# Optimization experiments

Hardware: AMD Instinct MI355X
Metric: run time of the kernel (lower is better)

## Reference

```python
import jax, jax.numpy as jnp
import numpy as np

DIM_X, DIM_Z, D_MODEL, N_HEADS, BATCH = 512, 256, 256, 8, 32


def sinusoidal_pe(seq_len, d_model):
    # standard sinusoidal table, rows indexed by position
    pos = np.arange(seq_len)[:, None].astype(np.float32)
    div = np.exp(np.arange(0, d_model, 2).astype(np.float32) * (-np.log(10000.0) / d_model))
    pe = np.zeros((seq_len, d_model), dtype=np.float32)
    pe[:, 0::2] = np.sin(pos * div)
    pe[:, 1::2] = np.cos(pos * div)
    return jnp.asarray(pe)


def setup_inputs() -> dict:
    key = jax.random.key(0)
    ks = jax.random.split(key, 5)
    state = jax.random.normal(ks[0], (BATCH, D_MODEL, DIM_X), dtype=jnp.float32)
    obs = jax.random.normal(ks[1], (BATCH, D_MODEL, DIM_Z), dtype=jnp.float32)
    Qp = jax.random.uniform(ks[2], (DIM_X, D_MODEL), dtype=jnp.float32)  # torch.rand init
    Wq = jax.random.normal(ks[3], (D_MODEL, D_MODEL), dtype=jnp.float32) / np.sqrt(D_MODEL)
    Wk = jax.random.normal(ks[4], (D_MODEL, D_MODEL), dtype=jnp.float32) / np.sqrt(D_MODEL)
    bq = jnp.zeros((D_MODEL,), dtype=jnp.float32)
    bk = jnp.zeros((D_MODEL,), dtype=jnp.float32)
    return {"state": state, "obs": obs, "Qp": Qp, "Wq": Wq, "bq": bq, "Wk": Wk, "bk": bk}


def reference(state, obs, Qp, Wq, bq, Wk, bk):
    bs, en, dim_x = state.shape
    dim_z = obs.shape[2]
    d_model = Qp.shape[1]
    h = N_HEADS
    hd = d_model // h
    S = dim_x + dim_z

    # mean-center over the ensemble axis
    A = state - jnp.mean(state, axis=1, keepdims=True)   # [bs, en, dim_x]
    Y = obs - jnp.mean(obs, axis=1, keepdims=True)       # [bs, en, dim_z]
    A = jnp.transpose(A, (2, 0, 1))                      # [dim_x, bs, en]
    Y = jnp.transpose(Y, (2, 0, 1))                      # [dim_z, bs, en]

    # positional encoding: batch_first=True quirk -> PE indexed along axis 1 (the bs axis)
    pe = sinusoidal_pe(bs, d_model)[None, :, :]          # [1, bs, d_model]
    query = Qp[:, None, :] + pe                          # [dim_x, bs, d_model] (broadcast of repeat)
    xy = jnp.concatenate([A, Y], axis=0) + pe            # [S, bs, d_model]

    # multi-head attention weights (V / out-proj do not affect returned quantities)
    q = (query @ Wq.T + bq).reshape(dim_x, bs, h, hd)
    k = (xy @ Wk.T + bk).reshape(S, bs, h, hd)
    scores = jnp.einsum('lbhd,sbhd->bhls', q, k) / np.sqrt(hd)  # [bs, h, dim_x, S]

    # fixed structured mask: eye(dim_x) | bottom-padded eye(dim_z)
    p1 = jnp.eye(dim_x, dtype=bool)
    p2 = jnp.concatenate([jnp.zeros((dim_x - dim_z, dim_z), dtype=bool),
                          jnp.eye(dim_z, dtype=bool)], axis=0)
    allow = jnp.concatenate([p1, p2], axis=1)            # [dim_x, S]
    scores = jnp.where(allow[None, None], scores, -jnp.inf)
    atten = jnp.mean(jax.nn.softmax(scores, axis=-1), axis=1)  # average over heads -> [bs, dim_x, S]

    # weighted merge of the ORIGINAL (uncentered) state/obs
    merge = jnp.concatenate([jnp.transpose(state, (0, 2, 1)),
                             jnp.transpose(obs, (0, 2, 1))], axis=1)  # [bs, S, en]
    new_state = jnp.einsum('bls,bse->ble', atten, merge)              # [bs, dim_x, en]
    new_state = jnp.transpose(new_state, (0, 2, 1))                   # [bs, en, dim_x]
    return new_state, atten
```

## Files before the change

kernel.cpp:

```cpp
#include <hip/hip_runtime.h>
#include <stdint.h>
#include <math.h>


#define WS_P    0
#define WS_QWT  8192
#define WS_PQ   73728
#define WS_U    81920
#define WS_V    606208
#define WS_QPT  671744
#define WS_WQT  737280

typedef float vf4 __attribute__((ext_vector_type(4)));
__device__ __forceinline__ void nt_store4(float* p, float x, float y,
                                          float z, float w) {
  vf4 v; v.x = x; v.y = y; v.z = z; v.w = w;
  __builtin_nontemporal_store(v, (vf4*)p);
}

__global__ void __launch_bounds__(256)
k_tr(const float* __restrict__ Qp, const float* __restrict__ Wq,
     float* __restrict__ ws) {
  __shared__ float tile[32][33];
  int bid = blockIdx.x, t = threadIdx.x;
  const float* src; float* dst; int ti;
  if (bid < 64) { src = Qp + 65536; dst = ws + WS_QPT; ti = bid; }
  else          { src = Wq;         dst = ws + WS_WQT; ti = bid - 64; }
  int tr = ti >> 3, tc = ti & 7;
  int c = t & 31, r0 = t >> 5;
  #pragma unroll
  for (int k = 0; k < 4; ++k) {
    int r = r0 + (k << 3);
    tile[r][c] = src[(size_t)(tr * 32 + r) * 256 + tc * 32 + c];
  }
  __syncthreads();
  #pragma unroll
  for (int k = 0; k < 4; ++k) {
    int r = r0 + (k << 3);
    dst[(size_t)(tc * 32 + r) * 256 + tr * 32 + c] = tile[c][r];
  }
}

__global__ void __launch_bounds__(256)
k_pro(const float* __restrict__ Wq, float* __restrict__ ws) {
  int bid = blockIdx.x, t = threadIdx.x;
  __shared__ float lvec[256];
  const float* __restrict__ GT; float* dst;
  if (bid < 256) {
    int d = bid;
    lvec[t] = Wq[(size_t)d * 256 + t];
    GT = ws + WS_QPT; dst = ws + WS_QWT + d * 256;
  } else {
    int b = bid - 256;
    int k2 = t & ~1;
    float div = expf((float)k2 * (-9.210340371976184f / 256.f));
    float a = (float)b * div;
    lvec[t] = (t & 1) ? cosf(a) : sinf(a);
    GT = ws + WS_WQT; dst = ws + WS_PQ + b * 256;
  }
  __syncthreads();
  float acc = 0.f;
  #pragma unroll 8
  for (int e = 0; e < 256; ++e)
    acc += lvec[e] * GT[(e << 8) + t];
  dst[t] = acc;
}

__global__ void __launch_bounds__(256)
k_uv(const float* __restrict__ Wk, const float* __restrict__ bq,
     float* __restrict__ ws) {
  int bid = blockIdx.x, t = threadIdx.x;
  if (bid < 256) {
    int h = bid >> 5, e0 = (bid & 31) << 3;
    __shared__ float wk_s[32][9];
    {
      int d = t >> 3, i = t & 7;
      wk_s[d][i] = Wk[(size_t)(h * 32 + d) * 256 + e0 + i];
    }
    __syncthreads();
    float acc[8] = {0.f, 0.f, 0.f, 0.f, 0.f, 0.f, 0.f, 0.f};
    const float* __restrict__ Qw = ws + WS_QWT + t;
    #pragma unroll 4
    for (int d = 0; d < 32; ++d) {
      float q = Qw[((h << 5) + d) << 8];
      #pragma unroll
      for (int i = 0; i < 8; ++i) acc[i] += wk_s[d][i] * q;
    }
    float* Uh = ws + WS_U + (h << 16) + (size_t)e0 * 256;
    #pragma unroll
    for (int i = 0; i < 8; ++i) Uh[(size_t)i * 256 + t] = acc[i];
  } else {
    int idx = bid - 256, b = idx >> 3, h = idx & 7;
    float acc = 0.f;
#pragma unroll 8
    for (int dd = 0; dd < 32; ++dd) {
      int d = h * 32 + dd;
      acc += (ws[WS_PQ + b * 256 + d] + bq[d]) * Wk[(size_t)d * 256 + t];
    }
    ws[WS_V + ((b << 3) + h) * 256 + t] = acc;
  }
}

__global__ void __launch_bounds__(256)
k_delta(const float* __restrict__ state, const float* __restrict__ obs,
        float* __restrict__ ws, float* __restrict__ out) {
  int bid = blockIdx.x, t = threadIdx.x;
  if (bid < 256) {
    int b = bid >> 3, jt = (bid & 7) << 5;
    __shared__ float Xs[256][33];
    __shared__ float Vs[2048];
    __shared__ float pd[8][8][32];
    __shared__ float pw[8][8][32];
    __shared__ float px[8][32];
    __shared__ float pfin[32];
    {
      int es = t >> 3, jq = t & 7;
      const float* sp = state + (size_t)b * 131072 + 256 + jt + (jq << 2);
      const float* op = obs   + (size_t)b * 65536  + jt + (jq << 2);
      #pragma unroll
      for (int k = 0; k < 8; ++k) {
        int e = es + (k << 5);
        float4 s4 = *(const float4*)(sp + (size_t)e * 512);
        float4 o4 = *(const float4*)(op + (size_t)e * 256);
        float* xr = &Xs[e][jq << 2];
        xr[0] = s4.x - o4.x; xr[1] = s4.y - o4.y;
        xr[2] = s4.z - o4.z; xr[3] = s4.w - o4.w;
      }
      for (int i = t; i < 2048; i += 256) Vs[i] = ws[WS_V + (b << 11) + i];
    }
    __syncthreads();
    int j = t & 31, eg = t >> 5, e0 = eg << 5;
    {
      float ax = 0.f;
      #pragma unroll
      for (int ei = 0; ei < 32; ++ei) ax += Xs[e0 + ei][j];
      px[eg][j] = ax;
    }
    const float* __restrict__ Ub = ws + WS_U + jt + j;
    #pragma unroll
    for (int h = 0; h < 8; ++h) {
      float dacc = 0.f, wacc = 0.f;
      const float* __restrict__ Uh = Ub + (h << 16) + (e0 << 8);
      const float* __restrict__ Vh = Vs + (h << 8) + e0;
      #pragma unroll 16
      for (int ei = 0; ei < 32; ++ei) {
        float w = Uh[ei << 8] + Vh[ei];
        dacc += Xs[e0 + ei][j] * w;
        wacc += w;
      }
      pd[eg][h][j] = dacc;
      pw[eg][h][j] = wacc;
    }
    __syncthreads();
    int h2 = t >> 5, j2 = t & 31;
    float D = 0.f, W = 0.f, X = 0.f;
    #pragma unroll
    for (int g = 0; g < 8; ++g) {
      D += pd[g][h2][j2];
      W += pw[g][h2][j2];
      X += px[g][j2];
    }
    float delta = D - X * (1.f / 256.f) * W;
    float sig = 1.f / (1.f + __expf(-delta * 0.17677669529663687f));
    __syncthreads();
    px[h2][j2] = sig;
    __syncthreads();
    if (t < 32) {
      float acc = 0.f;
      #pragma unroll
      for (int h = 0; h < 8; ++h) acc += px[h][t];
      ws[WS_P + (b << 8) + jt + t] = acc;
      float p = acc * 0.125f;
      pfin[t] = p;
      int l = 256 + jt + t;
      size_t rb = 4194304 + (size_t)((b << 9) + l) * 768;
      int c1 = l >> 2, pos = l & 3;
      float v1[4] = {0.f, 0.f, 0.f, 0.f}; v1[pos] = p;
      nt_store4(out + rb + (c1 << 2), v1[0], v1[1], v1[2], v1[3]);
      float v2[4] = {0.f, 0.f, 0.f, 0.f}; v2[pos] = 1.f - p;
      nt_store4(out + rb + ((c1 + 64) << 2), v2[0], v2[1], v2[2], v2[3]);
    }
    __syncthreads();
    {
      int eb = t >> 3, j0 = (t & 7) << 2;
      const float* op2 = obs + (size_t)b * 65536 + jt + j0;
      float p0 = pfin[j0], p1 = pfin[j0 + 1], p2 = pfin[j0 + 2], p3 = pfin[j0 + 3];
      float* orow = out + (size_t)b * 131072 + 256 + jt + j0;
      #pragma unroll
      for (int k = 0; k < 8; ++k) {
        int e = eb + (k << 5);
        float4 o4 = *(const float4*)(op2 + (size_t)e * 256);
        const float* xr = &Xs[e][j0];
        nt_store4(orow + (size_t)e * 512,
                  o4.x + p0 * xr[0], o4.y + p1 * xr[1],
                  o4.z + p2 * xr[2], o4.w + p3 * xr[3]);
      }
    }
  } else if (bid < 2304) {
    int row = ((bid - 256) << 2) | (t >> 6);
    int c = t & 63;
    float4 sv = ((const float4*)(state + (size_t)row * 512))[c];
    nt_store4(out + (size_t)row * 512 + (c << 2), sv.x, sv.y, sv.z, sv.w);
  } else {
    int g4 = (bid - 2304) * 256 + t;
    int r = g4 / 192, c = g4 - r * 192;
    int b = r >> 9, l = r & 511;
    int s0 = c << 2;
    if (l < 256) {
      float v[4] = {0.f, 0.f, 0.f, 0.f};
      if (l >= s0 && l < s0 + 4) v[l - s0] = 1.0f;
      nt_store4(out + 4194304 + ((size_t)g4 << 2), v[0], v[1], v[2], v[3]);
    } else {
      int c1 = l >> 2;
      if (c != c1 && c != c1 + 64)
        nt_store4(out + 4194304 + ((size_t)g4 << 2), 0.f, 0.f, 0.f, 0.f);
    }
  }
}

extern "C" void kernel_launch(void* const* d_in, const int* in_sizes, int n_in,
                              void* d_out, int out_size, void* d_ws, size_t ws_size,
                              hipStream_t stream) {
  const float *state = nullptr, *obs = nullptr, *Qp = nullptr;
  const float *Wq = nullptr, *Wk = nullptr, *bq = nullptr, *bk = nullptr;
  for (int i = 0; i < n_in; ++i) {
    int s = in_sizes[i];
    const float* p = (const float*)d_in[i];
    if      (s == 4194304) state = p;
    else if (s == 2097152) obs = p;
    else if (s == 131072)  Qp = p;
    else if (s == 65536)   { if (!Wq) Wq = p; else Wk = p; }
    else if (s == 256)     { if (!bq) bq = p; else bk = p; }
  }
  (void)bk;
  float* out = (float*)d_out;
  float* ws  = (float*)d_ws;

  k_tr   <<<128,   256, 0, stream>>>(Qp, Wq, ws);
  k_pro  <<<288,   256, 0, stream>>>(Wq, ws);
  k_uv   <<<512,   256, 0, stream>>>(Wk, bq, ws);
  k_delta<<<14592, 256, 0, stream>>>(state, obs, ws, out);
}
```

Measured before the change: 123.7 us.

## Fuse transpose and projection prologue kernels into one tiled shared-memory GEMM kernel

Replaces the separate transpose kernel and the projection kernel with a single kernel that computes Wq·Qp^T and Wq·PE directly from row-major inputs using float4 shared-memory tiles, which removes one launch and the workspace transposes. It also drops an unused workspace store of the per-row probability sum in the main kernel. The prologue now runs on only 72 blocks, so the GPU is less filled during that step, but the cost is small next to the main kernel.

Result: faster. 118.8 us (median of 2 runs) (-4.0%).

```diff
diff --git a/kernel.cpp b/kernel.cpp
--- a/kernel.cpp
+++ b/kernel.cpp
@@ -8,8 +8,6 @@
 #define WS_PQ   73728
 #define WS_U    81920
 #define WS_V    606208
-#define WS_QPT  671744
-#define WS_WQT  737280
 
 typedef float vf4 __attribute__((ext_vector_type(4)));
 __device__ __forceinline__ void nt_store4(float* p, float x, float y,
@@ -19,51 +17,82 @@
 }
 
 __global__ void __launch_bounds__(256)
-k_tr(const float* __restrict__ Qp, const float* __restrict__ Wq,
+k_qw(const float* __restrict__ Qp, const float* __restrict__ Wq,
      float* __restrict__ ws) {
-  __shared__ float tile[32][33];
   int bid = blockIdx.x, t = threadIdx.x;
-  const float* src; float* dst; int ti;
-  if (bid < 64) { src = Qp + 65536; dst = ws + WS_QPT; ti = bid; }
-  else          { src = Wq;         dst = ws + WS_WQT; ti = bid - 64; }
-  int tr = ti >> 3, tc = ti & 7;
-  int c = t & 31, r0 = t >> 5;
-  #pragma unroll
-  for (int k = 0; k < 4; ++k) {
-    int r = r0 + (k << 3);
-    tile[r][c] = src[(size_t)(tr * 32 + r) * 256 + tc * 32 + c];
-  }
-  __syncthreads();
-  #pragma unroll
-  for (int k = 0; k < 4; ++k) {
-    int r = r0 + (k << 3);
-    dst[(size_t)(tc * 32 + r) * 256 + tr * 32 + c] = tile[c][r];
-  }
-}
-
-__global__ void __launch_bounds__(256)
-k_pro(const float* __restrict__ Wq, float* __restrict__ ws) {
-  int bid = blockIdx.x, t = threadIdx.x;
-  __shared__ float lvec[256];
-  const float* __restrict__ GT; float* dst;
-  if (bid < 256) {
-    int d = bid;
-    lvec[t] = Wq[(size_t)d * 256 + t];
-    GT = ws + WS_QPT; dst = ws + WS_QWT + d * 256;
+  if (bid < 64) {
+    __shared__ float wq_s[32][132];
+    __shared__ float qp_s[32][132];
+    int d0 = (bid >> 3) << 5, j0 = (bid & 7) << 5;
+    int j = t & 31, dq = t >> 5;
+    float acc[4] = {0.f, 0.f, 0.f, 0.f};
+    for (int ec = 0; ec < 256; ec += 128) {
+      #pragma unroll
+      for (int k = 0; k < 4; ++k) {
+        int i = (k << 8) + t;
+        int r = i >> 5, c4 = i & 31;
+        *(float4*)&wq_s[r][c4 << 2] =
+            *(const float4*)(Wq + (size_t)(d0 + r) * 256 + ec + (c4 << 2));
+        *(float4*)&qp_s[r][c4 << 2] =
+            *(const float4*)(Qp + 65536 + (size_t)(j0 + r) * 256 + ec + (c4 << 2));
+      }
+      __syncthreads();
+      #pragma unroll 8
+      for (int e4 = 0; e4 < 32; ++e4) {
+        float4 q = *(const float4*)&qp_s[j][e4 << 2];
+        #pragma unroll
+        for (int r = 0; r < 4; ++r) {
+          float4 w = *(const float4*)&wq_s[(dq << 2) + r][e4 << 2];
+          acc[r] += w.x * q.x + w.y * q.y + w.z * q.z + w.w * q.w;
+        }
+      }
+      __syncthreads();
+    }
+    #pragma unroll
+    for (int r = 0; r < 4; ++r)
+      ws[WS_QWT + (size_t)(d0 + (dq << 2) + r) * 256 + j0 + j] = acc[r];
   } else {
-    int b = bid - 256;
-    int k2 = t & ~1;
-    float div = expf((float)k2 * (-9.210340371976184f / 256.f));
-    float a = (float)b * div;
-    lvec[t] = (t & 1) ? cosf(a) : sinf(a);
-    GT = ws + WS_WQT; dst = ws + WS_PQ + b * 256;
-  }
-  __syncthreads();
-  float acc = 0.f;
-  #pragma unroll 8
-  for (int e = 0; e < 256; ++e)
-    acc += lvec[e] * GT[(e << 8) + t];
-  dst[t] = acc;
+    __shared__ float wq_s[32][132];
+    __shared__ float pe_s[32][132];
+    int d0 = (bid - 64) << 5;
+    int b = t & 31, dq = t >> 5;
+    float acc[4] = {0.f, 0.f, 0.f, 0.f};
+    for (int ec = 0; ec < 256; ec += 128) {
+      #pragma unroll
+      for (int k = 0; k < 4; ++k) {
+        int i = (k << 8) + t;
+        int r = i >> 5, c4 = i & 31;
+        *(float4*)&wq_s[r][c4 << 2] =
+            *(const float4*)(Wq + (size_t)(d0 + r) * 256 + ec + (c4 << 2));
+      }
+      {
+        int b2 = t >> 3, e0 = (t & 7) << 4;
+        #pragma unroll
+        for (int k = 0; k < 16; ++k) {
+          int e = e0 + k;
+          int ge = ec + e;
+          int k2 = ge & ~1;
+          float div = expf((float)k2 * (-9.210340371976184f / 256.f));
+          float a = (float)b2 * div;
+          pe_s[b2][e] = (ge & 1) ? cosf(a) : sinf(a);
+        }
+      }
+      __syncthreads();
+      #pragma unroll 8
+      for (int e4 = 0; e4 < 32; ++e4) {
+        float4 p = *(const float4*)&pe_s[b][e4 << 2];
+        #pragma unroll
+        for (int r = 0; r < 4; ++r) {
+          float4 w = *(const float4*)&wq_s[(dq << 2) + r][e4 << 2];
+          acc[r] += w.x * p.x + w.y * p.y + w.z * p.z + w.w * p.w;
+        }
+      }
+      __syncthreads();
+    }
+    #pragma unroll
+    for (int r = 0; r < 4; ++r)
+      ws[WS_PQ + b * 256 + d0 + (dq << 2) + r] = acc[r];
+  }
 }
 
 __global__ void __launch_bounds__(256)
@@ -169,7 +198,6 @@
       float acc = 0.f;
       #pragma unroll
       for (int h = 0; h < 8; ++h) acc += px[h][t];
-      ws[WS_P + (b << 8) + jt + t] = acc;
       float p = acc * 0.125f;
       pfin[t] = p;
       int l = 256 + jt + t;
@@ -236,8 +264,7 @@
   float* out = (float*)d_out;
   float* ws  = (float*)d_ws;
 
-  k_tr   <<<128,   256, 0, stream>>>(Qp, Wq, ws);
-  k_pro  <<<288,   256, 0, stream>>>(Wq, ws);
+  k_qw   <<<72,    256, 0, stream>>>(Qp, Wq, ws);
   k_uv   <<<512,   256, 0, stream>>>(Wk, bq, ws);
   k_delta<<<14592, 256, 0, stream>>>(state, obs, ws, out);
 }
```
